# Kernel tuning notes

Hardware: AMD Instinct MI355X
Metric: run time of the kernel (lower is better)

## Reference

```python
import jax, jax.numpy as jnp
import numpy as np

B, T, HW = 16, 64, 7
D = 768          # input_dim == base_dim
N = 12           # num_heads
C = D // N       # head_dim = 64
EPS = 1e-5


def layernorm(x, g, b):
    m = jnp.mean(x, axis=-1, keepdims=True)
    v = jnp.mean((x - m) ** 2, axis=-1, keepdims=True)
    return (x - m) * jax.lax.rsqrt(v + EPS) * g + b


def setup_inputs() -> dict:
    key = jax.random.key(0)
    ks = jax.random.split(key, 12)
    s = lambda k, shape: (jax.random.normal(k, shape, jnp.float32) * 0.02)
    return {
        "x": jax.random.normal(ks[0], (B, T, HW, HW, D), jnp.float32),
        "W_qkv": s(ks[1], (D, 3 * D)),                  # qkv_bias=False
        "Wpq": s(ks[2], (C, C, HW, HW)), "bpq": jnp.zeros((C,), jnp.float32),
        "Wpk": s(ks[3], (C, C, HW, HW)), "bpk": jnp.zeros((C,), jnp.float32),
        "Wpv": s(ks[4], (C, C, HW, HW)), "bpv": jnp.zeros((C,), jnp.float32),
        "g_q": jnp.ones((C,), jnp.float32), "be_q": jnp.zeros((C,), jnp.float32),
        "g_k": jnp.ones((C,), jnp.float32), "be_k": jnp.zeros((C,), jnp.float32),
        "g_v": jnp.ones((C,), jnp.float32), "be_v": jnp.zeros((C,), jnp.float32),
        "rel_pos_t": s(ks[5], (2 * T - 1, C)),          # (127, 64): matches dt, no interp
        "W_proj": s(ks[6], (D, D)), "b_proj": jnp.zeros((D,), jnp.float32),
    }


def reference(x, W_qkv, Wpq, bpq, Wpk, bpk, Wpv, bpv,
              g_q, be_q, g_k, be_k, g_v, be_v, rel_pos_t, W_proj, b_proj):
    b, t = x.shape[0], x.shape[1]
    # qkv projection -> (B,T,H,W,3,N,C)
    qkv = (x @ W_qkv).reshape(b, t, HW, HW, 3, N, C)
    q3, k3, v3 = qkv[..., 0, :, :], qkv[..., 1, :, :], qkv[..., 2, :, :]  # (B,T,H,W,N,C)
    # Conv3d kernel (1,7,7) on full 7x7 spatial == contraction over (h,w,c_in)
    q = jnp.einsum('bthwnc,dchw->bntd', q3, Wpq) + bpq   # (B,N,T,C)
    k = jnp.einsum('bthwnc,dchw->bntd', k3, Wpk) + bpk
    v = jnp.einsum('bthwnc,dchw->bntd', v3, Wpv) + bpv
    q = layernorm(q, g_q, be_q)
    k = layernorm(k, g_k, be_k)
    v = layernorm(v, g_v, be_v)
    scale = C ** -0.5
    attn = jnp.einsum('bntc,bnsc->bnts', q * scale, k)   # (B,N,T,T)
    # relative temporal position bias: gather table rows by distance, matmul with q
    dist = jnp.arange(t)[:, None] - jnp.arange(t)[None, :] + (t - 1)  # (T,T) in [0,2T-2]
    Rt = rel_pos_t[dist]                                  # (T,T,C)
    rel = jnp.einsum('bntc,tsc->bnts', q, Rt)
    attn = jax.nn.softmax(attn + rel, axis=-1)
    out = jnp.einsum('bnts,bnsc->bntc', attn, v) + q      # residual add of q
    out = out.transpose(0, 2, 1, 3).reshape(b, t, N * C)  # (B,T,D)
    return out @ W_proj + b_proj
```

## Files before the change

kernel.cpp:

```cpp
#include <hip/hip_runtime.h>


typedef __attribute__((ext_vector_type(8))) short bf16x8;
typedef __attribute__((ext_vector_type(4))) float f32x4;

#define AS1U(p) ((const __attribute__((address_space(1))) unsigned int*)(p))
#define AS3U(p) ((__attribute__((address_space(3))) unsigned int*)(p))

__device__ __forceinline__ unsigned short cvt_bf16(float x) {
  union { float f; unsigned int u; } v; v.f = x;
  unsigned int r = v.u + 0x7fffu + ((v.u >> 16) & 1u);
  return (unsigned short)(r >> 16);
}
__device__ __forceinline__ float bf2f(unsigned short h) {
  union { unsigned int u; float f; } v; v.u = ((unsigned int)h) << 16;
  return v.f;
}

__device__ __forceinline__ void wg_barrier() {
  asm volatile("" ::: "memory");
  __builtin_amdgcn_s_barrier();
  asm volatile("" ::: "memory");
}

__global__ __launch_bounds__(256) void cvt_x_k(const float* __restrict__ src,
                                               unsigned short* __restrict__ dst, int n8) {
  int i = blockIdx.x * 256 + threadIdx.x;
  if (i >= n8) return;
  const float4* s = (const float4*)src + (size_t)i * 2;
  float4 a = s[0], b = s[1];
  ushort4 r0 = { cvt_bf16(a.x), cvt_bf16(a.y), cvt_bf16(a.z), cvt_bf16(a.w) };
  ushort4 r1 = { cvt_bf16(b.x), cvt_bf16(b.y), cvt_bf16(b.z), cvt_bf16(b.w) };
  ushort4* d = (ushort4*)dst + (size_t)i * 2;
  d[0] = r0; d[1] = r1;
}

__global__ __launch_bounds__(256) void transpose_cvt_k(const float* __restrict__ src,
                                                       unsigned short* __restrict__ dst) {
  __shared__ float tl[32][33];
  int k0 = blockIdx.x * 32, n0 = blockIdx.y * 32;
  int tx = threadIdx.x & 31, ty = threadIdx.x >> 5;
#pragma unroll
  for (int r = 0; r < 32; r += 8)
    tl[ty + r][tx] = src[(size_t)(k0 + ty + r) * 2304 + n0 + tx];
  __syncthreads();
#pragma unroll
  for (int r = 0; r < 32; r += 8)
    dst[(size_t)(n0 + ty + r) * 768 + k0 + tx] = cvt_bf16(tl[tx][ty + r]);
}

__global__ __launch_bounds__(256) void wp_cvt_k(const float* __restrict__ src,
                                                unsigned short* __restrict__ dst) {
  int o = blockIdx.x * 256 + threadIdx.x;
  if (o >= 204800) return;
  int c = o & 63, d = (o >> 6) & 63, hw = o >> 12;
  dst[o] = (hw < 49) ? cvt_bf16(src[d * 3136 + c * 49 + hw]) : (unsigned short)0;
}

__global__ __launch_bounds__(256) void relp_cvt_k(const float* __restrict__ src,
                                                  unsigned short* __restrict__ dst) {
  int i = blockIdx.x * 256 + threadIdx.x;
  if (i >= 8192) return;
  dst[i] = (i < 8128) ? cvt_bf16(src[i]) : (unsigned short)0;
}

__global__ __launch_bounds__(512, 2) void gemm_qkv_8ph(
    const unsigned short* __restrict__ A, const unsigned short* __restrict__ Bt,
    unsigned short* __restrict__ Cb) {
  __shared__ unsigned short As[2][16384];
  __shared__ unsigned short Bs[2][16384];

  const int orig = blockIdx.x;
  const int xcd = orig & 7;
  const int lid = orig >> 3;
  const int wgid = (xcd < 4 ? xcd * 221 : 884 + (xcd - 4) * 220) + lid;
  const int mb = wgid / 9, nb = wgid % 9;
  const int m0 = mb * 256, n0 = nb * 256;
  const int K = 768;

  const int tid = threadIdx.x;
  const int wave = tid >> 6, lane = tid & 63;
  const int quad = lane >> 4, l16 = lane & 15;
  const int wr = wave >> 2, wc = wave & 3;
  const int x7 = l16 & 7;

  const int srow = tid >> 3;
  const int cs = (tid & 7) ^ (srow & 7);
  const unsigned short* Ag[4];
  const unsigned short* Bg[4];
#pragma unroll
  for (int l = 0; l < 4; ++l) {
    Ag[l] = A + (size_t)(m0 + l * 64 + srow) * K + cs * 8;
    Bg[l] = Bt + (size_t)(n0 + l * 64 + srow) * K + cs * 8;
  }
  const int ldst = wave * 512;

#define STAGE(buf, kt) do {                                                        \
    const int ko_ = (kt) * 64;                                                     \
    _Pragma("unroll")                                                              \
    for (int l_ = 0; l_ < 4; ++l_) {                                               \
      __builtin_amdgcn_global_load_lds(AS1U(Ag[l_] + ko_),                         \
          AS3U(&As[buf][l_ * 4096 + ldst]), 16, 0, 0);                             \
      __builtin_amdgcn_global_load_lds(AS1U(Bg[l_] + ko_),                         \
          AS3U(&Bs[buf][l_ * 4096 + ldst]), 16, 0, 0);                             \
    }                                                                              \
  } while (0)

#define LDA(buf, mi) do {                                                          \
    _Pragma("unroll")                                                              \
    for (int fi_ = 0; fi_ < 4; ++fi_) {                                            \
      const int row_ = wr * 128 + (mi) * 64 + fi_ * 16 + l16;                      \
      _Pragma("unroll")                                                            \
      for (int ks_ = 0; ks_ < 2; ++ks_)                                            \
        af[fi_][ks_] = *(const bf16x8*)&As[buf][row_ * 64 +                        \
            (((ks_ * 4 + quad) ^ x7) * 8)];                                        \
    }                                                                              \
  } while (0)

#define LDB(buf, nj) do {                                                          \
    _Pragma("unroll")                                                              \
    for (int fj_ = 0; fj_ < 2; ++fj_) {                                            \
      const int row_ = wc * 64 + (nj) * 32 + fj_ * 16 + l16;                       \
      _Pragma("unroll")                                                            \
      for (int ks_ = 0; ks_ < 2; ++ks_)                                            \
        bfv[nj][fj_][ks_] = *(const bf16x8*)&Bs[buf][row_ * 64 +                   \
            (((ks_ * 4 + quad) ^ x7) * 8)];                                        \
    }                                                                              \
  } while (0)

#define MFMAQ(mi, nj) do {                                                         \
    _Pragma("unroll")                                                              \
    for (int ks_ = 0; ks_ < 2; ++ks_)                                              \
      _Pragma("unroll")                                                            \
      for (int fi_ = 0; fi_ < 4; ++fi_)                                            \
        _Pragma("unroll")                                                          \
        for (int fj_ = 0; fj_ < 2; ++fj_)                                          \
          acc[(mi) * 4 + fi_][(nj) * 2 + fj_] =                                    \
              __builtin_amdgcn_mfma_f32_16x16x32_bf16(af[fi_][ks_],                \
                  bfv[nj][fj_][ks_], acc[(mi) * 4 + fi_][(nj) * 2 + fj_], 0, 0, 0);\
  } while (0)

#define ITER(cur, DO_STAGE, kt2, VMI) do {                                         \
    asm volatile("s_waitcnt vmcnt(" #VMI ")" ::: "memory");                        \
    wg_barrier();                                                                  \
                                                                           \
    LDA(cur, 0); LDB(cur, 0);                                                      \
    wg_barrier();                                                                  \
    __builtin_amdgcn_s_setprio(1); MFMAQ(0, 0); __builtin_amdgcn_s_setprio(0);     \
    wg_barrier();                                                                  \
                                                                           \
    LDB(cur, 1);                                                                   \
    wg_barrier();                                                                  \
    __builtin_amdgcn_s_setprio(1); MFMAQ(0, 1); __builtin_amdgcn_s_setprio(0);     \
    wg_barrier();                                                                  \
                                                                           \
    LDA(cur, 1);                                                                   \
    wg_barrier();                                                                  \
    __builtin_amdgcn_s_setprio(1); MFMAQ(1, 0); __builtin_amdgcn_s_setprio(0);     \
    wg_barrier();                                                                  \
             \
    if (DO_STAGE) STAGE(cur, kt2);                                                 \
    __builtin_amdgcn_s_setprio(1); MFMAQ(1, 1); __builtin_amdgcn_s_setprio(0);     \
    wg_barrier();                                                                  \
  } while (0)

  f32x4 acc[8][4];
#pragma unroll
  for (int i = 0; i < 8; ++i)
#pragma unroll
    for (int j = 0; j < 4; ++j) acc[i][j] = (f32x4){0.f, 0.f, 0.f, 0.f};
  bf16x8 af[4][2];
  bf16x8 bfv[2][2][2];

  STAGE(0, 0);
  STAGE(1, 1);

  for (int kt = 0; kt < 10; kt += 2) {
    ITER(0, true, kt + 2, 8);
    ITER(1, true, kt + 3, 8);
  }
  ITER(0, false, 0, 8);
  ITER(1, false, 0, 0);

#undef ITER
#undef MFMAQ
#undef LDB
#undef LDA
#undef STAGE

#pragma unroll
  for (int i = 0; i < 8; ++i)
#pragma unroll
    for (int j = 0; j < 4; ++j)
#pragma unroll
      for (int r = 0; r < 4; ++r) {
        int row = m0 + wr * 128 + i * 16 + quad * 4 + r;
        int col = n0 + wc * 64 + j * 16 + l16;
        Cb[(size_t)row * 2304 + col] = cvt_bf16(acc[i][j][r]);
      }
}

__global__ __launch_bounds__(256) void pool_ln_mfma_k(
    const unsigned short* __restrict__ qkvb, const unsigned short* __restrict__ WpTT,
    const float* __restrict__ bq, const float* __restrict__ bk, const float* __restrict__ bv,
    const float* __restrict__ gq, const float* __restrict__ gk, const float* __restrict__ gv,
    const float* __restrict__ beq, const float* __restrict__ bek, const float* __restrict__ bev,
    unsigned short* __restrict__ oq, unsigned short* __restrict__ ok_,
    unsigned short* __restrict__ ov) {
  __shared__ unsigned short As[64 * 128];
  __shared__ unsigned short Bs[64 * 128];
  __shared__ float Ln[64 * 65];
  __shared__ float mu_s[64], rs_s[64];

  const int n = blockIdx.x, p = blockIdx.y, b = blockIdx.z;
  const int tid = threadIdx.x;
  const int wave = tid >> 6, lane = tid & 63;
  const int quad = lane >> 4, l16 = lane & 15;
  const int wm = (wave >> 1) * 32, wn = (wave & 1) * 32;

  const int lr = lane >> 4, lg = lane & 15;
  const size_t abase = ((size_t)b * 3136) * 2304 + (size_t)p * 768 + (size_t)n * 64;
  const unsigned short* WpB = WpTT + (size_t)p * 204800;

  const unsigned short* pA[4];
  const unsigned short* pB[4];
#pragma unroll
  for (int q = 0; q < 4; ++q) {
    int r = wave * 16 + q * 4 + lr;
    int g = lg ^ (r & 15);
    pA[q] = qkvb + abase + (size_t)r * 112896 + (size_t)(g >> 3) * 2304 + (g & 7) * 8;
    pB[q] = WpB + (size_t)(g >> 3) * 4096 + r * 64 + (g & 7) * 8;
  }

  f32x4 acc[2][2];
#pragma unroll
  for (int i = 0; i < 2; ++i)
#pragma unroll
    for (int j = 0; j < 2; ++j) acc[i][j] = (f32x4){0.f, 0.f, 0.f, 0.f};

  for (int it = 0; it < 25; ++it) {
    const size_t offA = (size_t)it * 4608;
    const size_t offB = (size_t)it * 8192;
#pragma unroll
    for (int q = 0; q < 4; ++q) {
      __builtin_amdgcn_global_load_lds(AS1U(pA[q] + offA), AS3U(&As[(wave * 16 + q * 4) * 128]), 16, 0, 0);
      __builtin_amdgcn_global_load_lds(AS1U(pB[q] + offB), AS3U(&Bs[(wave * 16 + q * 4) * 128]), 16, 0, 0);
    }
    __syncthreads();
    bf16x8 af[2][4], bfr[2][4];
#pragma unroll
    for (int f = 0; f < 2; ++f) {
      int ra = wm + f * 16 + l16;
      int rb = wn + f * 16 + l16;
#pragma unroll
      for (int ki = 0; ki < 4; ++ki) {
        af[f][ki]  = *(const bf16x8*)&As[ra * 128 + (((ki * 4 + quad) ^ (ra & 15)) * 8)];
        bfr[f][ki] = *(const bf16x8*)&Bs[rb * 128 + (((ki * 4 + quad) ^ (rb & 15)) * 8)];
      }
    }
#pragma unroll
    for (int ki = 0; ki < 4; ++ki)
#pragma unroll
      for (int i = 0; i < 2; ++i)
#pragma unroll
        for (int j = 0; j < 2; ++j)
          acc[i][j] = __builtin_amdgcn_mfma_f32_16x16x32_bf16(af[i][ki], bfr[j][ki], acc[i][j], 0, 0, 0);
    __syncthreads();
  }

  const float* bias = (p == 0) ? bq : (p == 1) ? bk : bv;
  const float* g    = (p == 0) ? gq : (p == 1) ? gk : gv;
  const float* be   = (p == 0) ? beq : (p == 1) ? bek : bev;
  unsigned short* outp = (p == 0) ? oq : (p == 1) ? ok_ : ov;

#pragma unroll
  for (int i = 0; i < 2; ++i)
#pragma unroll
    for (int j = 0; j < 2; ++j)
#pragma unroll
      for (int r = 0; r < 4; ++r) {
        int t = wm + i * 16 + quad * 4 + r;
        int d = wn + j * 16 + l16;
        Ln[t * 65 + d] = acc[i][j][r] + bias[d];
      }
  __syncthreads();
  if (tid < 64) {
    float s = 0.f;
#pragma unroll 8
    for (int c = 0; c < 64; ++c) s += Ln[tid * 65 + c];
    float m = s * (1.f / 64.f);
    float v2 = 0.f;
#pragma unroll 8
    for (int c = 0; c < 64; ++c) { float dl = Ln[tid * 65 + c] - m; v2 += dl * dl; }
    mu_s[tid] = m;
    rs_s[tid] = rsqrtf(v2 * (1.f / 64.f) + 1e-5f);
  }
  __syncthreads();
  {
    int t = tid >> 2, d0 = (tid & 3) * 16;
    float m = mu_s[t], rv = rs_s[t];
    unsigned short ob[16];
#pragma unroll
    for (int j = 0; j < 16; ++j)
      ob[j] = cvt_bf16((Ln[t * 65 + d0 + j] - m) * rv * g[d0 + j] + be[d0 + j]);
    unsigned short* dst = outp + ((size_t)(b * 12 + n) * 64 + t) * 64 + d0;
    *(uint4*)dst = *(uint4*)ob;
    *(uint4*)(dst + 8) = *(uint4*)(ob + 8);
  }
}

__global__ __launch_bounds__(256) void attn_mfma_k(
    const unsigned short* __restrict__ qp, const unsigned short* __restrict__ kp,
    const unsigned short* __restrict__ vp, const unsigned short* __restrict__ relb,
    float* __restrict__ aout) {
  __shared__ unsigned short qs[64 * 64];
  __shared__ unsigned short ks[64 * 64];
  __shared__ unsigned short vt[64 * 64];
  __shared__ unsigned short rs[128 * 64];
  __shared__ float Gs[64 * 128];
  __shared__ unsigned short Ps[64 * 64];

  const int n = blockIdx.x, b = blockIdx.y;
  const int tid = threadIdx.x;
  const size_t base = ((size_t)b * 12 + n) * 4096;

  for (int i = tid; i < 512; i += 256) {
    ((uint4*)qs)[i] = ((const uint4*)(qp + base))[i];
    ((uint4*)ks)[i] = ((const uint4*)(kp + base))[i];
  }
  for (int i = tid; i < 1024; i += 256)
    ((uint4*)rs)[i] = ((const uint4*)relb)[i];
  {
    int s = tid >> 2, c0 = (tid & 3) * 16;
    unsigned short tmp[16];
    *(uint4*)tmp = *(const uint4*)(vp + base + s * 64 + c0);
    *(uint4*)(tmp + 8) = *(const uint4*)(vp + base + s * 64 + c0 + 8);
#pragma unroll
    for (int i = 0; i < 16; ++i) vt[(c0 + i) * 64 + s] = tmp[i];
  }
  __syncthreads();

  const int wave = tid >> 6, lane = tid & 63;
  const int quad = lane >> 4, l16 = lane & 15;
  const int tm = wave * 16;

  bf16x8 aq[2];
  aq[0] = *(const bf16x8*)&qs[(tm + l16) * 64 + quad * 8];
  aq[1] = *(const bf16x8*)&qs[(tm + l16) * 64 + quad * 8 + 32];

  f32x4 accqk[4], accg[8];
#pragma unroll
  for (int j = 0; j < 4; ++j) accqk[j] = (f32x4){0.f, 0.f, 0.f, 0.f};
#pragma unroll
  for (int j = 0; j < 8; ++j) accg[j] = (f32x4){0.f, 0.f, 0.f, 0.f};

#pragma unroll
  for (int ki = 0; ki < 2; ++ki) {
#pragma unroll
    for (int j = 0; j < 4; ++j) {
      bf16x8 bk = *(const bf16x8*)&ks[(j * 16 + l16) * 64 + quad * 8 + ki * 32];
      accqk[j] = __builtin_amdgcn_mfma_f32_16x16x32_bf16(aq[ki], bk, accqk[j], 0, 0, 0);
    }
#pragma unroll
    for (int j = 0; j < 8; ++j) {
      bf16x8 br = *(const bf16x8*)&rs[(j * 16 + l16) * 64 + quad * 8 + ki * 32];
      accg[j] = __builtin_amdgcn_mfma_f32_16x16x32_bf16(aq[ki], br, accg[j], 0, 0, 0);
    }
  }
#pragma unroll
  for (int j = 0; j < 8; ++j)
#pragma unroll
    for (int r = 0; r < 4; ++r)
      Gs[(tm + quad * 4 + r) * 128 + j * 16 + l16] = accg[j][r];
  __syncthreads();

#pragma unroll
  for (int r = 0; r < 4; ++r) {
    int t = tm + quad * 4 + r;
    float sv[4];
#pragma unroll
    for (int j = 0; j < 4; ++j) {
      int s = j * 16 + l16;
      sv[j] = 0.125f * accqk[j][r] + Gs[t * 128 + (t + 63 - s)];
    }
    float m = fmaxf(fmaxf(sv[0], sv[1]), fmaxf(sv[2], sv[3]));
    m = fmaxf(m, __shfl_xor(m, 1));
    m = fmaxf(m, __shfl_xor(m, 2));
    m = fmaxf(m, __shfl_xor(m, 4));
    m = fmaxf(m, __shfl_xor(m, 8));
    float e[4], sum = 0.f;
#pragma unroll
    for (int j = 0; j < 4; ++j) { e[j] = __expf(sv[j] - m); sum += e[j]; }
    sum += __shfl_xor(sum, 1);
    sum += __shfl_xor(sum, 2);
    sum += __shfl_xor(sum, 4);
    sum += __shfl_xor(sum, 8);
    float inv = 1.f / sum;
#pragma unroll
    for (int j = 0; j < 4; ++j)
      Ps[t * 64 + j * 16 + l16] = cvt_bf16(e[j] * inv);
  }
  __syncthreads();

  bf16x8 ap[2];
  ap[0] = *(const bf16x8*)&Ps[(tm + l16) * 64 + quad * 8];
  ap[1] = *(const bf16x8*)&Ps[(tm + l16) * 64 + quad * 8 + 32];
  f32x4 acco[4];
#pragma unroll
  for (int j = 0; j < 4; ++j) acco[j] = (f32x4){0.f, 0.f, 0.f, 0.f};
#pragma unroll
  for (int ki = 0; ki < 2; ++ki)
#pragma unroll
    for (int j = 0; j < 4; ++j) {
      bf16x8 bv = *(const bf16x8*)&vt[(j * 16 + l16) * 64 + quad * 8 + ki * 32];
      acco[j] = __builtin_amdgcn_mfma_f32_16x16x32_bf16(ap[ki], bv, acco[j], 0, 0, 0);
    }
#pragma unroll
  for (int j = 0; j < 4; ++j)
#pragma unroll
    for (int r = 0; r < 4; ++r) {
      int t = tm + quad * 4 + r;
      int c = j * 16 + l16;
      float o = acco[j][r] + bf2f(qs[t * 64 + c]);
      aout[((size_t)b * 64 + t) * 768 + n * 64 + c] = o;
    }
}

__global__ __launch_bounds__(256) void gemm_f32_k(
    const float* __restrict__ A, const float* __restrict__ Bm,
    const float* __restrict__ bias, float* __restrict__ Cm,
    int M, int Nn, int K) {
  __shared__ float As[16][68];
  __shared__ float Bs[16][64];
  const int tid = threadIdx.x;
  const int ty = tid >> 4, tx = tid & 15;
  const int m0 = blockIdx.y * 64, n0 = blockIdx.x * 64;

  const int la_m = tid >> 2;
  const int la_k = (tid & 3) << 2;
  const int lb_k = tid >> 4;
  const int lb_n = (tid & 15) << 2;

  const float* Ap = A + (size_t)(m0 + la_m) * K + la_k;
  const float* Bp = Bm + (size_t)lb_k * Nn + n0 + lb_n;

  float acc[4][4];
#pragma unroll
  for (int i = 0; i < 4; ++i)
#pragma unroll
    for (int j = 0; j < 4; ++j) acc[i][j] = 0.f;

  for (int k0 = 0; k0 < K; k0 += 16) {
    float4 av = *(const float4*)(Ap + k0);
    float4 bv = *(const float4*)(Bp + (size_t)k0 * Nn);
    As[la_k + 0][la_m] = av.x;
    As[la_k + 1][la_m] = av.y;
    As[la_k + 2][la_m] = av.z;
    As[la_k + 3][la_m] = av.w;
    *(float4*)&Bs[lb_k][lb_n] = bv;
    __syncthreads();
#pragma unroll
    for (int kk = 0; kk < 16; ++kk) {
      float af[4], bf[4];
      *(float4*)af = *(const float4*)&As[kk][ty << 2];
      *(float4*)bf = *(const float4*)&Bs[kk][tx << 2];
#pragma unroll
      for (int i = 0; i < 4; ++i)
#pragma unroll
        for (int j = 0; j < 4; ++j) acc[i][j] += af[i] * bf[j];
    }
    __syncthreads();
  }

  float bb[4] = {0.f, 0.f, 0.f, 0.f};
  if (bias) {
#pragma unroll
    for (int j = 0; j < 4; ++j) bb[j] = bias[n0 + (tx << 2) + j];
  }
#pragma unroll
  for (int i = 0; i < 4; ++i) {
    float4 o;
    o.x = acc[i][0] + bb[0];
    o.y = acc[i][1] + bb[1];
    o.z = acc[i][2] + bb[2];
    o.w = acc[i][3] + bb[3];
    *(float4*)(Cm + (size_t)(m0 + (ty << 2) + i) * Nn + n0 + (tx << 2)) = o;
  }
}

extern "C" void kernel_launch(void* const* d_in, const int* in_sizes, int n_in,
                              void* d_out, int out_size, void* d_ws, size_t ws_size,
                              hipStream_t stream) {
  const float* x     = (const float*)d_in[0];
  const float* Wqkv  = (const float*)d_in[1];
  const float* Wpq   = (const float*)d_in[2];
  const float* bpq   = (const float*)d_in[3];
  const float* Wpk   = (const float*)d_in[4];
  const float* bpk   = (const float*)d_in[5];
  const float* Wpv   = (const float*)d_in[6];
  const float* bpv   = (const float*)d_in[7];
  const float* gq    = (const float*)d_in[8];
  const float* beq   = (const float*)d_in[9];
  const float* gk    = (const float*)d_in[10];
  const float* bek   = (const float*)d_in[11];
  const float* gv    = (const float*)d_in[12];
  const float* bev   = (const float*)d_in[13];
  const float* relp  = (const float*)d_in[14];
  const float* Wproj = (const float*)d_in[15];
  const float* bproj = (const float*)d_in[16];
  float* out = (float*)d_out;

  unsigned short* u = (unsigned short*)d_ws;
  unsigned short* xbf   = u;
  unsigned short* qkvbf = u + 38535168ull;
  unsigned short* WqkvT = u + 154140672ull;
  unsigned short* WpTT  = u + 155910144ull;
  unsigned short* relb  = u + 156524544ull;
  unsigned short* qpb   = u + 156532736ull;
  unsigned short* kpb   = u + 157319168ull;
  unsigned short* vpb   = u + 158105600ull;
  float* aout = (float*)(u + 158892032ull);

  cvt_x_k<<<18816, 256, 0, stream>>>(x, xbf, 4816896);
  transpose_cvt_k<<<dim3(24, 72), 256, 0, stream>>>(Wqkv, WqkvT);
  wp_cvt_k<<<800, 256, 0, stream>>>(Wpq, WpTT);
  wp_cvt_k<<<800, 256, 0, stream>>>(Wpk, WpTT + 204800);
  wp_cvt_k<<<800, 256, 0, stream>>>(Wpv, WpTT + 409600);
  relp_cvt_k<<<32, 256, 0, stream>>>(relp, relb);

  gemm_qkv_8ph<<<1764, 512, 0, stream>>>(xbf, WqkvT, qkvbf);

  pool_ln_mfma_k<<<dim3(12, 3, 16), 256, 0, stream>>>(
      qkvbf, WpTT, bpq, bpk, bpv, gq, gk, gv, beq, bek, bev, qpb, kpb, vpb);

  attn_mfma_k<<<dim3(12, 16), 256, 0, stream>>>(qpb, kpb, vpb, relb, aout);

  gemm_f32_k<<<dim3(12, 16), 256, 0, stream>>>(aout, Wproj, bproj, out, 1024, 768, 768);
}
```

Before: 614.6 us.

## Double-buffer pool GEMM loads and merge small weight conversion kernels

The pooling MFMA kernel moves to a two-stage LDS ping-pong. The next tile's global-to-LDS loads are issued before the current tile is computed, with a partial vmcnt wait, so load latency overlaps with MFMA work. The LDS arrays are unioned into one buffer that is reused for the LayerNorm stage. Separately, four tiny conversion launches are merged into one kernel to cut launch overhead. The double buffering raises LDS use per block, which may lower occupancy.

```diff
diff --git a/kernel.cpp b/kernel.cpp
--- a/kernel.cpp
+++ b/kernel.cpp
@@ -49,19 +49,23 @@
     dst[(size_t)(n0 + ty + r) * 768 + k0 + tx] = cvt_bf16(tl[tx][ty + r]);
 }
 
-__global__ __launch_bounds__(256) void wp_cvt_k(const float* __restrict__ src,
-                                                unsigned short* __restrict__ dst) {
-  int o = blockIdx.x * 256 + threadIdx.x;
-  if (o >= 204800) return;
-  int c = o & 63, d = (o >> 6) & 63, hw = o >> 12;
-  dst[o] = (hw < 49) ? cvt_bf16(src[d * 3136 + c * 49 + hw]) : (unsigned short)0;
-}
-
-__global__ __launch_bounds__(256) void relp_cvt_k(const float* __restrict__ src,
-                                                  unsigned short* __restrict__ dst) {
-  int i = blockIdx.x * 256 + threadIdx.x;
-  if (i >= 8192) return;
-  dst[i] = (i < 8128) ? cvt_bf16(src[i]) : (unsigned short)0;
+__global__ __launch_bounds__(256) void prep_cvt_k(
+    const float* __restrict__ Wpq, const float* __restrict__ Wpk,
+    const float* __restrict__ Wpv, const float* __restrict__ relp,
+    unsigned short* __restrict__ WpTT, unsigned short* __restrict__ relb) {
+  int bid = blockIdx.x;
+  if (bid < 2400) {
+    int p = bid / 800;
+    const float* src = (p == 0) ? Wpq : (p == 1) ? Wpk : Wpv;
+    unsigned short* dst = WpTT + (size_t)p * 204800;
+    int o = (bid - p * 800) * 256 + threadIdx.x;
+    if (o >= 204800) return;
+    int c = o & 63, d = (o >> 6) & 63, hw = o >> 12;
+    dst[o] = (hw < 49) ? cvt_bf16(src[d * 3136 + c * 49 + hw]) : (unsigned short)0;
+  } else {
+    int i = (bid - 2400) * 256 + threadIdx.x;
+    relb[i] = (i < 8128) ? cvt_bf16(relp[i]) : (unsigned short)0;
+  }
 }
 
 __global__ __launch_bounds__(512, 2) void gemm_qkv_8ph(
@@ -207,10 +211,10 @@
     const float* __restrict__ beq, const float* __restrict__ bek, const float* __restrict__ bev,
     unsigned short* __restrict__ oq, unsigned short* __restrict__ ok_,
     unsigned short* __restrict__ ov) {
-  __shared__ unsigned short As[64 * 128];
-  __shared__ unsigned short Bs[64 * 128];
-  __shared__ float Ln[64 * 65];
+  __shared__ float smem_f[16384];
   __shared__ float mu_s[64], rs_s[64];
+  unsigned short* AB = (unsigned short*)smem_f;
+  float* Ln = smem_f;
 
   const int n = blockIdx.x, p = blockIdx.y, b = blockIdx.z;
   const int tid = threadIdx.x;
@@ -232,41 +236,72 @@
     pB[q] = WpB + (size_t)(g >> 3) * 4096 + r * 64 + (g & 7) * 8;
   }
 
+#define PSTAGE(buf, it) do {                                                       \
+    const size_t offA_ = (size_t)(it) * 4608;                                      \
+    const size_t offB_ = (size_t)(it) * 8192;                                      \
+    unsigned short* Ad_ = AB + (buf) * 8192;                                       \
+    unsigned short* Bd_ = AB + 16384 + (buf) * 8192;                               \
+    _Pragma("unroll")                                                              \
+    for (int q_ = 0; q_ < 4; ++q_) {                                               \
+      __builtin_amdgcn_global_load_lds(AS1U(pA[q_] + offA_),                       \
+          AS3U(&Ad_[(wave * 16 + q_ * 4) * 128]), 16, 0, 0);                       \
+      __builtin_amdgcn_global_load_lds(AS1U(pB[q_] + offB_),                       \
+          AS3U(&Bd_[(wave * 16 + q_ * 4) * 128]), 16, 0, 0);                       \
+    }                                                                              \
+  } while (0)
+
+#define PCOMPUTE(buf) do {                                                         \
+    const unsigned short* Ad_ = AB + (buf) * 8192;                                 \
+    const unsigned short* Bd_ = AB + 16384 + (buf) * 8192;                         \
+    bf16x8 af_[2][4], bf_[2][4];                                                   \
+    _Pragma("unroll")                                                              \
+    for (int f_ = 0; f_ < 2; ++f_) {                                               \
+      int ra_ = wm + f_ * 16 + l16;                                                \
+      int rb_ = wn + f_ * 16 + l16;                                                \
+      _Pragma("unroll")                                                            \
+      for (int ki_ = 0; ki_ < 4; ++ki_) {                                          \
+        af_[f_][ki_] = *(const bf16x8*)&Ad_[ra_ * 128 +                            \
+            (((ki_ * 4 + quad) ^ (ra_ & 15)) * 8)];                                \
+        bf_[f_][ki_] = *(const bf16x8*)&Bd_[rb_ * 128 +                            \
+            (((ki_ * 4 + quad) ^ (rb_ & 15)) * 8)];                                \
+      }                                                                            \
+    }                                                                              \
+    _Pragma("unroll")                                                              \
+    for (int ki_ = 0; ki_ < 4; ++ki_)                                              \
+      _Pragma("unroll")                                                            \
+      for (int i_ = 0; i_ < 2; ++i_)                                               \
+        _Pragma("unroll")                                                          \
+        for (int j_ = 0; j_ < 2; ++j_)                                             \
+          acc[i_][j_] = __builtin_amdgcn_mfma_f32_16x16x32_bf16(                   \
+              af_[i_][ki_], bf_[j_][ki_], acc[i_][j_], 0, 0, 0);                   \
+  } while (0)
+
   f32x4 acc[2][2];
 #pragma unroll
   for (int i = 0; i < 2; ++i)
 #pragma unroll
     for (int j = 0; j < 2; ++j) acc[i][j] = (f32x4){0.f, 0.f, 0.f, 0.f};
 
-  for (int it = 0; it < 25; ++it) {
-    const size_t offA = (size_t)it * 4608;
-    const size_t offB = (size_t)it * 8192;
-#pragma unroll
-    for (int q = 0; q < 4; ++q) {
-      __builtin_amdgcn_global_load_lds(AS1U(pA[q] + offA), AS3U(&As[(wave * 16 + q * 4) * 128]), 16, 0, 0);
-      __builtin_amdgcn_global_load_lds(AS1U(pB[q] + offB), AS3U(&Bs[(wave * 16 + q * 4) * 128]), 16, 0, 0);
-    }
-    __syncthreads();
-    bf16x8 af[2][4], bfr[2][4];
-#pragma unroll
-    for (int f = 0; f < 2; ++f) {
-      int ra = wm + f * 16 + l16;
-      int rb = wn + f * 16 + l16;
-#pragma unroll
-      for (int ki = 0; ki < 4; ++ki) {
-        af[f][ki]  = *(const bf16x8*)&As[ra * 128 + (((ki * 4 + quad) ^ (ra & 15)) * 8)];
-        bfr[f][ki] = *(const bf16x8*)&Bs[rb * 128 + (((ki * 4 + quad) ^ (rb & 15)) * 8)];
-      }
-    }
-#pragma unroll
-    for (int ki = 0; ki < 4; ++ki)
-#pragma unroll
-      for (int i = 0; i < 2; ++i)
-#pragma unroll
-        for (int j = 0; j < 2; ++j)
-          acc[i][j] = __builtin_amdgcn_mfma_f32_16x16x32_bf16(af[i][ki], bfr[j][ki], acc[i][j], 0, 0, 0);
-    __syncthreads();
-  }
+  PSTAGE(0, 0);
+  for (int it2 = 0; it2 < 24; it2 += 2) {
+    PSTAGE(1, it2 + 1);
+    asm volatile("s_waitcnt vmcnt(8)" ::: "memory");
+    wg_barrier();
+    PCOMPUTE(0);
+    wg_barrier();
+    PSTAGE(0, it2 + 2);
+    asm volatile("s_waitcnt vmcnt(8)" ::: "memory");
+    wg_barrier();
+    PCOMPUTE(1);
+    wg_barrier();
+  }
+  asm volatile("s_waitcnt vmcnt(0)" ::: "memory");
+  wg_barrier();
+  PCOMPUTE(0);
+  __syncthreads();
+
+#undef PCOMPUTE
+#undef PSTAGE
 
   const float* bias = (p == 0) ? bq : (p == 1) ? bk : bv;
   const float* g    = (p == 0) ? gq : (p == 1) ? gk : gv;
@@ -523,10 +558,7 @@
 
   cvt_x_k<<<18816, 256, 0, stream>>>(x, xbf, 4816896);
   transpose_cvt_k<<<dim3(24, 72), 256, 0, stream>>>(Wqkv, WqkvT);
-  wp_cvt_k<<<800, 256, 0, stream>>>(Wpq, WpTT);
-  wp_cvt_k<<<800, 256, 0, stream>>>(Wpk, WpTT + 204800);
-  wp_cvt_k<<<800, 256, 0, stream>>>(Wpv, WpTT + 409600);
-  relp_cvt_k<<<32, 256, 0, stream>>>(relp, relb);
+  prep_cvt_k<<<2432, 256, 0, stream>>>(Wpq, Wpk, Wpv, relp, WpTT, relb);
 
   gemm_qkv_8ph<<<1764, 512, 0, stream>>>(xbf, WqkvT, qkvbf);
 
```

New measurement: 617.2 us. No clear change (+0.4%).
